# Kernel tuning notes

Measured on AMD Instinct MI355X. Metric: run time of the kernel, lower is better.

The kernel has to match this reference:

```python
import jax, jax.numpy as jnp
import numpy as np
from jax import lax

HW = 256

def setup_inputs() -> dict:
    key = jax.random.key(0)
    k1, k2, k3 = jax.random.split(key, 3)
    B, C = 8, 64
    x1 = jax.random.normal(k1, (B, C, HW, HW), dtype=jnp.float32)
    x2 = jax.random.normal(k2, (B, C, HW, HW), dtype=jnp.float32)
    w = jnp.ones((1, 1, 3, 3), dtype=jnp.float32) / 9.0  # fixed box filter
    b = jax.random.normal(k3, (1,), dtype=jnp.float32) * 0.1  # conv bias
    return {"x1": x1, "x2": x2, "w": w, "b": b}

def _box_conv(y, w, b):
    # y: [B,1,H,W] ; 3x3 conv, stride 1, pad 1, plus bias
    out = lax.conv_general_dilated(
        y, w, window_strides=(1, 1), padding=[(1, 1), (1, 1)],
        dimension_numbers=("NCHW", "OIHW", "NCHW"))
    return out + b.reshape(1, -1, 1, 1)

def reference(x1, x2, w, b):
    # channel-wise L1 norm -> [B,1,H,W]
    n1 = jnp.sum(jnp.abs(x1), axis=-3).reshape(-1, 1, HW, HW)
    n2 = jnp.sum(jnp.abs(x2), axis=-3).reshape(-1, 1, HW, HW)
    c1 = _box_conv(n1, w, b)
    c2 = _box_conv(n2, w, b)
    denom = c1 + c2
    return x1 * c1 / denom + x2 * c2 / denom
```

## Files before the change

kernel.cpp:

```cpp
#include <hip/hip_runtime.h>

#define HWD 256
#define HW2 (HWD * HWD)
#define NB 8
#define NC 64
#define PLANE4 (HW2 / 4)

typedef float floatx4 __attribute__((ext_vector_type(4)));

__global__ void norms_kernel(const float* __restrict__ x1,
                             const float* __restrict__ x2,
                             float* __restrict__ n1,
                             float* __restrict__ n2) {
    const int s = threadIdx.x & 63;
    const int g = threadIdx.x >> 6;
    const int blk = blockIdx.x;
    const int b = blk >> 8;
    const int p = ((blk & 255) << 6) + s;

    const size_t base = (size_t)b * NC * PLANE4 + (size_t)g * 16 * PLANE4 + p;
    const float4* x1v = (const float4*)x1 + base;
    const float4* x2v = (const float4*)x2 + base;

    float4 a1 = make_float4(0.f, 0.f, 0.f, 0.f);
    float4 a2 = make_float4(0.f, 0.f, 0.f, 0.f);

#pragma unroll
    for (int c0 = 0; c0 < 16; c0 += 4) {
        float4 v1[4], v2[4];
#pragma unroll
        for (int j = 0; j < 4; ++j) v1[j] = x1v[(size_t)(c0 + j) * PLANE4];
#pragma unroll
        for (int j = 0; j < 4; ++j) v2[j] = x2v[(size_t)(c0 + j) * PLANE4];
#pragma unroll
        for (int j = 0; j < 4; ++j) {
            a1.x += fabsf(v1[j].x); a1.y += fabsf(v1[j].y);
            a1.z += fabsf(v1[j].z); a1.w += fabsf(v1[j].w);
            a2.x += fabsf(v2[j].x); a2.y += fabsf(v2[j].y);
            a2.z += fabsf(v2[j].z); a2.w += fabsf(v2[j].w);
        }
    }

    __shared__ float4 l1[4][64];
    __shared__ float4 l2[4][64];
    l1[g][s] = a1;
    l2[g][s] = a2;
    __syncthreads();

    const size_t oidx = (size_t)b * PLANE4 + p;
    if (g == 0) {
        float4 r0 = l1[0][s], r1 = l1[1][s], r2 = l1[2][s], r3 = l1[3][s];
        float4 o;
        o.x = (r0.x + r1.x) + (r2.x + r3.x);
        o.y = (r0.y + r1.y) + (r2.y + r3.y);
        o.z = (r0.z + r1.z) + (r2.z + r3.z);
        o.w = (r0.w + r1.w) + (r2.w + r3.w);
        ((float4*)n1)[oidx] = o;
    } else if (g == 1) {
        float4 r0 = l2[0][s], r1 = l2[1][s], r2 = l2[2][s], r3 = l2[3][s];
        float4 o;
        o.x = (r0.x + r1.x) + (r2.x + r3.x);
        o.y = (r0.y + r1.y) + (r2.y + r3.y);
        o.z = (r0.z + r1.z) + (r2.z + r3.z);
        o.w = (r0.w + r1.w) + (r2.w + r3.w);
        ((float4*)n2)[oidx] = o;
    }
}

__global__ void conv_ratio_kernel(const float* __restrict__ n1,
                                  const float* __restrict__ n2,
                                  const float* __restrict__ w,
                                  const float* __restrict__ bias,
                                  float* __restrict__ r) {
    int t = blockIdx.x * blockDim.x + threadIdx.x;
    int b = t >> 14;
    int sp = t & ((HW2 / 4) - 1);
    int y = sp >> 6;
    int x0 = (sp & 63) << 2;

    const float* p1 = n1 + (size_t)b * HW2;
    const float* p2 = n2 + (size_t)b * HW2;

    float o1[4] = {0.f, 0.f, 0.f, 0.f};
    float o2[4] = {0.f, 0.f, 0.f, 0.f};

#pragma unroll
    for (int dy = -1; dy <= 1; ++dy) {
        int yy = y + dy;
        if (yy < 0 || yy >= HWD) continue;
        const float* r1 = p1 + yy * HWD;
        const float* r2 = p2 + yy * HWD;
        float4 m1 = *(const float4*)(r1 + x0);
        float4 m2 = *(const float4*)(r2 + x0);
        float e1[6], e2[6];
        e1[0] = (x0 > 0) ? r1[x0 - 1] : 0.f;
        e2[0] = (x0 > 0) ? r2[x0 - 1] : 0.f;
        e1[1] = m1.x; e1[2] = m1.y; e1[3] = m1.z; e1[4] = m1.w;
        e2[1] = m2.x; e2[2] = m2.y; e2[3] = m2.z; e2[4] = m2.w;
        e1[5] = (x0 + 4 < HWD) ? r1[x0 + 4] : 0.f;
        e2[5] = (x0 + 4 < HWD) ? r2[x0 + 4] : 0.f;
        const float* wr = w + (dy + 1) * 3;
#pragma unroll
        for (int j = 0; j < 4; ++j) {
#pragma unroll
            for (int k = 0; k < 3; ++k) {
                o1[j] += wr[k] * e1[j + k];
                o2[j] += wr[k] * e2[j + k];
            }
        }
    }

    float bv = bias[0];
    float4 out;
    {
        float c1 = o1[0] + bv, c2 = o2[0] + bv; out.x = c1 / (c1 + c2);
    }
    {
        float c1 = o1[1] + bv, c2 = o2[1] + bv; out.y = c1 / (c1 + c2);
    }
    {
        float c1 = o1[2] + bv, c2 = o2[2] + bv; out.z = c1 / (c1 + c2);
    }
    {
        float c1 = o1[3] + bv, c2 = o2[3] + bv; out.w = c1 / (c1 + c2);
    }
    ((float4*)r)[t] = out;
}

#define BLEND_BLOCKS 8192
#define BLEND_STRIDE ((size_t)BLEND_BLOCKS * 256)

__global__ void blend_kernel(const float* __restrict__ x1,
                             const float* __restrict__ x2,
                             const float* __restrict__ r,
                             float* __restrict__ out) {
    size_t idx = (size_t)blockIdx.x * 256 + threadIdx.x;
    const float4* x1v = (const float4*)x1;
    const float4* x2v = (const float4*)x2;
    const float4* rv4 = (const float4*)r;
    floatx4* ov = (floatx4*)out;

#pragma unroll
    for (int k = 0; k < 4; ++k) {
        size_t i = idx + (size_t)k * BLEND_STRIDE;
        int b = (int)(i >> 20);
        int p = (int)(i & (PLANE4 - 1));
        float4 rv = rv4[((size_t)b << 14) + p];
        float4 v1 = x1v[i];
        float4 v2 = x2v[i];
        floatx4 o;
        o.x = v1.x * rv.x + v2.x * (1.f - rv.x);
        o.y = v1.y * rv.y + v2.y * (1.f - rv.y);
        o.z = v1.z * rv.z + v2.z * (1.f - rv.z);
        o.w = v1.w * rv.w + v2.w * (1.f - rv.w);
        __builtin_nontemporal_store(o, ov + i);
    }
}

extern "C" void kernel_launch(void* const* d_in, const int* in_sizes, int n_in,
                              void* d_out, int out_size, void* d_ws, size_t ws_size,
                              hipStream_t stream) {
    const float* x1 = (const float*)d_in[0];
    const float* x2 = (const float*)d_in[1];
    const float* w  = (const float*)d_in[2];
    const float* bv = (const float*)d_in[3];
    float* out = (float*)d_out;

    float* n1 = (float*)d_ws;
    float* n2 = n1 + (size_t)NB * HW2;
    float* r  = n2 + (size_t)NB * HW2;

    const int block = 256;

    norms_kernel<<<NB * (PLANE4 / 64), block, 0, stream>>>(x1, x2, n1, n2);
    conv_ratio_kernel<<<NB * HW2 / 4 / block, block, 0, stream>>>(n1, n2, w, bv, r);
    blend_kernel<<<BLEND_BLOCKS, block, 0, stream>>>(x1, x2, r, out);
}
```

Before: 361.4 us.

## Split channel-norm reduction into partial-sum kernel plus separate combine pass

Replaces the single norms kernel, which reduced 64 channels through shared memory in each block, with a two-stage scheme. The first stage has each block handle one channel group of 16 over 512 pixel float4s, rotating the channel start per block and batching 8 loads before the accumulates. It writes partial sums into the output buffer, used as scratch. A second small kernel sums the four partials per image. This removes the shared-memory sync and is meant to raise memory-level parallelism, at the cost of an extra launch and extra scratch traffic.

```diff
diff --git a/kernel.cpp b/kernel.cpp
--- a/kernel.cpp
+++ b/kernel.cpp
@@ -8,63 +8,91 @@
 
 typedef float floatx4 __attribute__((ext_vector_type(4)));
 
-__global__ void norms_kernel(const float* __restrict__ x1,
-                             const float* __restrict__ x2,
-                             float* __restrict__ n1,
-                             float* __restrict__ n2) {
-    const int s = threadIdx.x & 63;
-    const int g = threadIdx.x >> 6;
-    const int blk = blockIdx.x;
-    const int b = blk >> 8;
-    const int p = ((blk & 255) << 6) + s;
+#define PSTRIDE ((size_t)NB * PLANE4)
 
-    const size_t base = (size_t)b * NC * PLANE4 + (size_t)g * 16 * PLANE4 + p;
-    const float4* x1v = (const float4*)x1 + base;
-    const float4* x2v = (const float4*)x2 + base;
+__device__ inline void acc_abs(float4& a, const float4 v) {
+    a.x += fabsf(v.x); a.y += fabsf(v.y);
+    a.z += fabsf(v.z); a.w += fabsf(v.w);
+}
 
-    float4 a1 = make_float4(0.f, 0.f, 0.f, 0.f);
-    float4 a2 = make_float4(0.f, 0.f, 0.f, 0.f);
+__global__ __launch_bounds__(256, 4)
+void norms_partial_kernel(const float* __restrict__ x1,
+                          const float* __restrict__ x2,
+                          float* __restrict__ scratch) {
+    const int tid  = threadIdx.x;
+    const int blk  = blockIdx.x;
+    const int tile = blk & 31;
+    const int cg   = (blk >> 5) & 3;
+    const int b    = blk >> 7;
+    const int rot  = blk & 7;
+
+    const int p0 = tile * 512 + tid;
+
+    const size_t ibase = ((size_t)(b * NC + cg * 16)) * PLANE4 + p0;
+    const float4* x1v = (const float4*)x1 + ibase;
+    const float4* x2v = (const float4*)x2 + ibase;
+
+    float4 a1a = make_float4(0.f, 0.f, 0.f, 0.f);
+    float4 a1b = make_float4(0.f, 0.f, 0.f, 0.f);
+    float4 a2a = make_float4(0.f, 0.f, 0.f, 0.f);
+    float4 a2b = make_float4(0.f, 0.f, 0.f, 0.f);
 
 #pragma unroll
-    for (int c0 = 0; c0 < 16; c0 += 4) {
-        float4 v1[4], v2[4];
-#pragma unroll
-        for (int j = 0; j < 4; ++j) v1[j] = x1v[(size_t)(c0 + j) * PLANE4];
-#pragma unroll
-        for (int j = 0; j < 4; ++j) v2[j] = x2v[(size_t)(c0 + j) * PLANE4];
-#pragma unroll
-        for (int j = 0; j < 4; ++j) {
-            a1.x += fabsf(v1[j].x); a1.y += fabsf(v1[j].y);
-            a1.z += fabsf(v1[j].z); a1.w += fabsf(v1[j].w);
-            a2.x += fabsf(v2[j].x); a2.y += fabsf(v2[j].y);
-            a2.z += fabsf(v2[j].z); a2.w += fabsf(v2[j].w);
-        }
+    for (int pr = 0; pr < 8; ++pr) {
+        const int c = ((pr + rot) & 7) * 2;
+        const size_t o0 = (size_t)c * PLANE4;
+        const size_t o1 = o0 + PLANE4;
+        float4 v0 = x1v[o0];
+        float4 v1 = x1v[o0 + 256];
+        float4 v2 = x2v[o0];
+        float4 v3 = x2v[o0 + 256];
+        float4 v4 = x1v[o1];
+        float4 v5 = x1v[o1 + 256];
+        float4 v6 = x2v[o1];
+        float4 v7 = x2v[o1 + 256];
+        __builtin_amdgcn_sched_barrier(0);
+        acc_abs(a1a, v0); acc_abs(a1b, v1);
+        acc_abs(a2a, v2); acc_abs(a2b, v3);
+        acc_abs(a1a, v4); acc_abs(a1b, v5);
+        acc_abs(a2a, v6); acc_abs(a2b, v7);
     }
 
-    __shared__ float4 l1[4][64];
-    __shared__ float4 l2[4][64];
-    l1[g][s] = a1;
-    l2[g][s] = a2;
-    __syncthreads();
+    float4* P1 = (float4*)scratch + (size_t)cg * PSTRIDE + (size_t)b * PLANE4;
+    float4* P2 = P1 + 4 * PSTRIDE;
+    P1[p0]       = a1a;
+    P1[p0 + 256] = a1b;
+    P2[p0]       = a2a;
+    P2[p0 + 256] = a2b;
+}
 
-    const size_t oidx = (size_t)b * PLANE4 + p;
-    if (g == 0) {
-        float4 r0 = l1[0][s], r1 = l1[1][s], r2 = l1[2][s], r3 = l1[3][s];
-        float4 o;
-        o.x = (r0.x + r1.x) + (r2.x + r3.x);
-        o.y = (r0.y + r1.y) + (r2.y + r3.y);
-        o.z = (r0.z + r1.z) + (r2.z + r3.z);
-        o.w = (r0.w + r1.w) + (r2.w + r3.w);
-        ((float4*)n1)[oidx] = o;
-    } else if (g == 1) {
-        float4 r0 = l2[0][s], r1 = l2[1][s], r2 = l2[2][s], r3 = l2[3][s];
-        float4 o;
-        o.x = (r0.x + r1.x) + (r2.x + r3.x);
-        o.y = (r0.y + r1.y) + (r2.y + r3.y);
-        o.z = (r0.z + r1.z) + (r2.z + r3.z);
-        o.w = (r0.w + r1.w) + (r2.w + r3.w);
-        ((float4*)n2)[oidx] = o;
-    }
+__global__ void sum_partials_kernel(const float* __restrict__ scratch,
+                                    float* __restrict__ n1,
+                                    float* __restrict__ n2) {
+    const size_t t = (size_t)blockIdx.x * 256 + threadIdx.x;
+    const float4* P = (const float4*)scratch;
+
+    float4 u0 = P[0 * PSTRIDE + t];
+    float4 u1 = P[1 * PSTRIDE + t];
+    float4 u2 = P[2 * PSTRIDE + t];
+    float4 u3 = P[3 * PSTRIDE + t];
+    float4 s1;
+    s1.x = (u0.x + u1.x) + (u2.x + u3.x);
+    s1.y = (u0.y + u1.y) + (u2.y + u3.y);
+    s1.z = (u0.z + u1.z) + (u2.z + u3.z);
+    s1.w = (u0.w + u1.w) + (u2.w + u3.w);
+
+    float4 w0 = P[4 * PSTRIDE + t];
+    float4 w1 = P[5 * PSTRIDE + t];
+    float4 w2 = P[6 * PSTRIDE + t];
+    float4 w3 = P[7 * PSTRIDE + t];
+    float4 s2;
+    s2.x = (w0.x + w1.x) + (w2.x + w3.x);
+    s2.y = (w0.y + w1.y) + (w2.y + w3.y);
+    s2.z = (w0.z + w1.z) + (w2.z + w3.z);
+    s2.w = (w0.w + w1.w) + (w2.w + w3.w);
+
+    ((float4*)n1)[t] = s1;
+    ((float4*)n2)[t] = s2;
 }
 
 __global__ void conv_ratio_kernel(const float* __restrict__ n1,
@@ -112,18 +140,10 @@
 
     float bv = bias[0];
     float4 out;
-    {
-        float c1 = o1[0] + bv, c2 = o2[0] + bv; out.x = c1 / (c1 + c2);
-    }
-    {
-        float c1 = o1[1] + bv, c2 = o2[1] + bv; out.y = c1 / (c1 + c2);
-    }
-    {
-        float c1 = o1[2] + bv, c2 = o2[2] + bv; out.z = c1 / (c1 + c2);
-    }
-    {
-        float c1 = o1[3] + bv, c2 = o2[3] + bv; out.w = c1 / (c1 + c2);
-    }
+    { float c1 = o1[0] + bv, c2 = o2[0] + bv; out.x = c1 / (c1 + c2); }
+    { float c1 = o1[1] + bv, c2 = o2[1] + bv; out.y = c1 / (c1 + c2); }
+    { float c1 = o1[2] + bv, c2 = o2[2] + bv; out.z = c1 / (c1 + c2); }
+    { float c1 = o1[3] + bv, c2 = o2[3] + bv; out.w = c1 / (c1 + c2); }
     ((float4*)r)[t] = out;
 }
 
@@ -172,7 +192,8 @@
 
     const int block = 256;
 
-    norms_kernel<<<NB * (PLANE4 / 64), block, 0, stream>>>(x1, x2, n1, n2);
+    norms_partial_kernel<<<1024, block, 0, stream>>>(x1, x2, out);
+    sum_partials_kernel<<<512, block, 0, stream>>>(out, n1, n2);
     conv_ratio_kernel<<<NB * HW2 / 4 / block, block, 0, stream>>>(n1, n2, w, bv, r);
     blend_kernel<<<BLEND_BLOCKS, block, 0, stream>>>(x1, x2, r, out);
 }
```

After: 373.3 us. +3.3%, slower.
